# Optimization experiments

Hardware: AMD Instinct MI355X
Metric: run time of the kernel (lower is better)

Reference implementation:

```python
import jax, jax.numpy as jnp
import numpy as np


def setup_inputs() -> dict:
    key = jax.random.key(0)
    k1, k2 = jax.random.split(key)
    T, D, E = 8192, 4096, 64  # tokens, model_dim, num_experts
    x = jax.random.normal(k1, (T, D), dtype=jnp.float32)
    wg = jax.random.normal(k2, (E, D), dtype=jnp.float32) * (1.0 / np.sqrt(D))
    return {"x": x, "wg": wg}


def reference(x, wg):
    # gate logits: nn.Linear(model_dim, num_experts, bias=False) in fp32
    logits = jnp.einsum('td,ed->te', x.astype(jnp.float32), wg)  # [T, E]
    gates = jax.nn.softmax(logits, axis=1)                        # [T, E]
    # top1gating (eval mode: no noise): argmax over gates
    indices1_s = jnp.argmax(gates, axis=1)                        # [T] int
    # gates = (gates * one_hot(indices1_s)).sum(dim=1) == gather of the max gate
    gates1_s = jnp.take_along_axis(gates, indices1_s[:, None], axis=1)[:, 0]  # [T]
    return indices1_s, gates1_s
```

## Files before the change

kernel.cpp:

```cpp
#include <hip/hip_runtime.h>

typedef __attribute__((ext_vector_type(8))) short bf16x8;
typedef __attribute__((ext_vector_type(4))) float f32x4;

constexpr int TN = 8192;
constexpr int DN = 4096;
constexpr int EN = 64;

constexpr int BM = 32;
constexpr int NS = DN / 32;
constexpr int NT = 16;

__device__ __forceinline__ unsigned short f2bf(float f) {
    unsigned u = __builtin_bit_cast(unsigned, f);
    u += 0x7FFFu + ((u >> 16) & 1u);
    return (unsigned short)(u >> 16);
}
__device__ __forceinline__ float bf2f(unsigned short h) {
    unsigned u = ((unsigned)h) << 16;
    return __builtin_bit_cast(float, u);
}

__global__ __launch_bounds__(256)
void wg_frag_kernel(const float* __restrict__ wg, unsigned short* __restrict__ BF) {
    const int gid = blockIdx.x * 256 + threadIdx.x;
    const int l  = gid & 63;
    const int et = (gid >> 6) & 3;
    const int s  = (gid >> 8) & (NS - 1);
    const int p  = gid >> 15;
    const int e  = et * 16 + (l & 15);
    const int k  = s * 32 + (l >> 4) * 8;

    const float* src = wg + (size_t)e * DN + k;
    float4 v0 = *reinterpret_cast<const float4*>(src);
    float4 v1 = *reinterpret_cast<const float4*>(src + 4);
    float f[8] = {v0.x, v0.y, v0.z, v0.w, v1.x, v1.y, v1.z, v1.w};
    unsigned short o[8];
#pragma unroll
    for (int j = 0; j < 8; ++j) {
        unsigned short h = f2bf(f[j]);
        o[j] = p ? f2bf(f[j] - bf2f(h)) : h;
    }
    unsigned short* dst = BF + (((size_t)p * NS + s) * 4 + et) * 512 + (size_t)l * 8;
    *reinterpret_cast<ushort4*>(dst)     = make_ushort4(o[0], o[1], o[2], o[3]);
    *reinterpret_cast<ushort4*>(dst + 4) = make_ushort4(o[4], o[5], o[6], o[7]);
}

__global__ __launch_bounds__(512, 2)
void gate_fused_kernel(const float* __restrict__ x,
                       const unsigned short* __restrict__ BF,
                       float* __restrict__ out) {
    __shared__ float L[8][BM][68];

    const int tid  = threadIdx.x;
    const int lane = tid & 63;
    const int w    = tid >> 6;
    const int kq   = w & 3;
    const int kh   = w >> 2;
    const int r0   = blockIdx.x * BM;

    const int fr  = lane & 15;
    const int fko = (lane >> 4) * 8;

    const float* xa = x + (size_t)(r0 + fr) * DN + fko;

    f32x4 acc[2][4] = {};

    float4 XA0[2][2], XA1[2][2];
    bf16x8 B0[8], B1[8];

    auto loadA = [&](float4 (&XA)[2][2], int t) {
        const int s = kh * 64 + t * 4 + kq;
        const float* p = xa + s * 32;
#pragma unroll
        for (int rh = 0; rh < 2; ++rh) {
            const float* pr = p + (size_t)rh * 16 * DN;
            XA[rh][0] = *reinterpret_cast<const float4*>(pr);
            XA[rh][1] = *reinterpret_cast<const float4*>(pr + 4);
        }
    };
    auto loadB = [&](bf16x8 (&B)[8], int t) {
        const int s = kh * 64 + t * 4 + kq;
        const unsigned short* bp = BF + (size_t)s * 2048 + (size_t)lane * 8;
#pragma unroll
        for (int et = 0; et < 4; ++et)
            B[et] = *reinterpret_cast<const bf16x8*>(bp + et * 512);
#pragma unroll
        for (int et = 0; et < 4; ++et)
            B[4 + et] = *reinterpret_cast<const bf16x8*>(bp + (size_t)NS * 2048 + et * 512);
    };
    auto compute = [&](float4 (&XA)[2][2], bf16x8 (&B)[8]) {
        bf16x8 ah[2], al[2];
#pragma unroll
        for (int rh = 0; rh < 2; ++rh) {
            float f[8] = {XA[rh][0].x, XA[rh][0].y, XA[rh][0].z, XA[rh][0].w,
                          XA[rh][1].x, XA[rh][1].y, XA[rh][1].z, XA[rh][1].w};
#pragma unroll
            for (int j = 0; j < 8; ++j) {
                unsigned short hh = f2bf(f[j]);
                ah[rh][j] = (short)hh;
                al[rh][j] = (short)f2bf(f[j] - bf2f(hh));
            }
        }
#pragma unroll
        for (int et = 0; et < 4; ++et)
#pragma unroll
            for (int rh = 0; rh < 2; ++rh) {
                acc[rh][et] = __builtin_amdgcn_mfma_f32_16x16x32_bf16(ah[rh], B[et],     acc[rh][et], 0, 0, 0);
                acc[rh][et] = __builtin_amdgcn_mfma_f32_16x16x32_bf16(al[rh], B[et],     acc[rh][et], 0, 0, 0);
                acc[rh][et] = __builtin_amdgcn_mfma_f32_16x16x32_bf16(ah[rh], B[4 + et], acc[rh][et], 0, 0, 0);
                acc[rh][et] = __builtin_amdgcn_mfma_f32_16x16x32_bf16(al[rh], B[4 + et], acc[rh][et], 0, 0, 0);
            }
    };

    loadA(XA0, 0);
    loadB(B0, 0);
#pragma unroll 2
    for (int t = 0; t < NT; t += 2) {
        if (t + 1 < NT) { loadA(XA1, t + 1); loadB(B1, t + 1); }
        compute(XA0, B0);
        if (t + 2 < NT) { loadA(XA0, t + 2); loadB(B0, t + 2); }
        compute(XA1, B1);
    }

#pragma unroll
    for (int rh = 0; rh < 2; ++rh)
#pragma unroll
        for (int et = 0; et < 4; ++et)
#pragma unroll
            for (int r = 0; r < 4; ++r)
                L[w][rh * 16 + (lane >> 4) * 4 + r][et * 16 + fr] = acc[rh][et][r];
    __syncthreads();

    {
        const int row = tid >> 4;
        const int eg  = tid & 15;
        float v[4];
#pragma unroll
        for (int j = 0; j < 4; ++j) {
            float s = L[0][row][eg * 4 + j];
#pragma unroll
            for (int q = 1; q < 8; ++q) s += L[q][row][eg * 4 + j];
            v[j] = s;
        }
        float m = v[0];
        int idx = eg * 4;
#pragma unroll
        for (int j = 1; j < 4; ++j)
            if (v[j] > m) { m = v[j]; idx = eg * 4 + j; }
#pragma unroll
        for (int d = 1; d < 16; d <<= 1) {
            float om = __shfl_xor(m, d);
            int   oi = __shfl_xor(idx, d);
            if (om > m || (om == m && oi < idx)) { m = om; idx = oi; }
        }
        float s = 0.0f;
#pragma unroll
        for (int j = 0; j < 4; ++j) s += __expf(v[j] - m);
#pragma unroll
        for (int d = 1; d < 16; d <<= 1) s += __shfl_xor(s, d);
        if (eg == 0) {
            out[r0 + row]      = (float)idx;
            out[TN + r0 + row] = 1.0f / s;
        }
    }
}

extern "C" void kernel_launch(void* const* d_in, const int* in_sizes, int n_in,
                              void* d_out, int out_size, void* d_ws, size_t ws_size,
                              hipStream_t stream) {
    const float* x  = (const float*)d_in[0];
    const float* wg = (const float*)d_in[1];
    float* out = (float*)d_out;

    unsigned short* BF = (unsigned short*)d_ws;

    wg_frag_kernel<<<dim3(256), dim3(256), 0, stream>>>(wg, BF);
    gate_fused_kernel<<<dim3(TN / BM), dim3(512), 0, stream>>>(x, BF, out);
}
```

Measured before the change: 38.26 us.

## Split gate GEMM over K into partials with a separate top-1 softmax kernel

The fused gate kernel becomes two kernels. A GEMM kernel uses 256 threads and 16-row tiles, splits the K dimension in two across blocks, and writes partial logits to workspace. A second kernel sums the partials per row and does argmax plus softmax normalisation. The aim is more, smaller blocks for better occupancy and latency hiding while streaming x. The cost is an extra launch, a partial-logit round trip, doubled reads of the weight fragments, and B loads that are no longer double-buffered. The KSPLIT=1 fallback only covers half of K, so it would give wrong results if it ever ran.

```diff
diff --git a/kernel.cpp b/kernel.cpp
--- a/kernel.cpp
+++ b/kernel.cpp
@@ -7,7 +7,7 @@
 constexpr int DN = 4096;
 constexpr int EN = 64;
 
-constexpr int BM = 32;
+constexpr int BM = 16;
 constexpr int NS = DN / 32;
 constexpr int NT = 16;
 
@@ -46,41 +46,38 @@
     *reinterpret_cast<ushort4*>(dst + 4) = make_ushort4(o[4], o[5], o[6], o[7]);
 }
 
-__global__ __launch_bounds__(512, 2)
-void gate_fused_kernel(const float* __restrict__ x,
-                       const unsigned short* __restrict__ BF,
-                       float* __restrict__ out) {
-    __shared__ float L[8][BM][68];
+template <int KSPLIT>
+__global__ __launch_bounds__(256, 4)
+void gate_gemm_kernel(const float* __restrict__ x,
+                      const unsigned short* __restrict__ BF,
+                      float* __restrict__ part) {
+    __shared__ float L[4][BM][68];
 
     const int tid  = threadIdx.x;
     const int lane = tid & 63;
     const int w    = tid >> 6;
-    const int kq   = w & 3;
-    const int kh   = w >> 2;
-    const int r0   = blockIdx.x * BM;
+    const int rt   = blockIdx.x >> (KSPLIT - 1);
+    const int ks   = blockIdx.x & (KSPLIT - 1);
+    const int r0   = rt * BM;
+    const int sbase = ks * (NS / KSPLIT);
 
     const int fr  = lane & 15;
     const int fko = (lane >> 4) * 8;
 
     const float* xa = x + (size_t)(r0 + fr) * DN + fko;
 
-    f32x4 acc[2][4] = {};
+    f32x4 acc[4] = {};
 
-    float4 XA0[2][2], XA1[2][2];
-    bf16x8 B0[8], B1[8];
+    float4 XA0[2], XA1[2];
+    bf16x8 B[8];
 
-    auto loadA = [&](float4 (&XA)[2][2], int t) {
-        const int s = kh * 64 + t * 4 + kq;
-        const float* p = xa + s * 32;
-#pragma unroll
-        for (int rh = 0; rh < 2; ++rh) {
-            const float* pr = p + (size_t)rh * 16 * DN;
-            XA[rh][0] = *reinterpret_cast<const float4*>(pr);
-            XA[rh][1] = *reinterpret_cast<const float4*>(pr + 4);
-        }
+    auto loadA = [&](float4 (&XA)[2], int t) {
+        const float* p = xa + (size_t)(sbase + t * 4 + w) * 32;
+        XA[0] = *reinterpret_cast<const float4*>(p);
+        XA[1] = *reinterpret_cast<const float4*>(p + 4);
     };
-    auto loadB = [&](bf16x8 (&B)[8], int t) {
-        const int s = kh * 64 + t * 4 + kq;
+    auto loadB = [&](int t) {
+        const int s = sbase + t * 4 + w;
         const unsigned short* bp = BF + (size_t)s * 2048 + (size_t)lane * 8;
 #pragma unroll
         for (int et = 0; et < 4; ++et)
@@ -89,47 +86,43 @@
         for (int et = 0; et < 4; ++et)
             B[4 + et] = *reinterpret_cast<const bf16x8*>(bp + (size_t)NS * 2048 + et * 512);
     };
-    auto compute = [&](float4 (&XA)[2][2], bf16x8 (&B)[8]) {
-        bf16x8 ah[2], al[2];
+    auto compute = [&](float4 (&XA)[2]) {
+        float f[8] = {XA[0].x, XA[0].y, XA[0].z, XA[0].w,
+                      XA[1].x, XA[1].y, XA[1].z, XA[1].w};
+        bf16x8 ah, al;
 #pragma unroll
-        for (int rh = 0; rh < 2; ++rh) {
-            float f[8] = {XA[rh][0].x, XA[rh][0].y, XA[rh][0].z, XA[rh][0].w,
-                          XA[rh][1].x, XA[rh][1].y, XA[rh][1].z, XA[rh][1].w};
-#pragma unroll
-            for (int j = 0; j < 8; ++j) {
-                unsigned short hh = f2bf(f[j]);
-                ah[rh][j] = (short)hh;
-                al[rh][j] = (short)f2bf(f[j] - bf2f(hh));
-            }
+        for (int j = 0; j < 8; ++j) {
+            unsigned short hh = f2bf(f[j]);
+            ah[j] = (short)hh;
+            al[j] = (short)f2bf(f[j] - bf2f(hh));
         }
 #pragma unroll
-        for (int et = 0; et < 4; ++et)
-#pragma unroll
-            for (int rh = 0; rh < 2; ++rh) {
-                acc[rh][et] = __builtin_amdgcn_mfma_f32_16x16x32_bf16(ah[rh], B[et],     acc[rh][et], 0, 0, 0);
-                acc[rh][et] = __builtin_amdgcn_mfma_f32_16x16x32_bf16(al[rh], B[et],     acc[rh][et], 0, 0, 0);
-                acc[rh][et] = __builtin_amdgcn_mfma_f32_16x16x32_bf16(ah[rh], B[4 + et], acc[rh][et], 0, 0, 0);
-                acc[rh][et] = __builtin_amdgcn_mfma_f32_16x16x32_bf16(al[rh], B[4 + et], acc[rh][et], 0, 0, 0);
-            }
+        for (int et = 0; et < 4; ++et) {
+            acc[et] = __builtin_amdgcn_mfma_f32_16x16x32_bf16(ah, B[et],     acc[et], 0, 0, 0);
+            acc[et] = __builtin_amdgcn_mfma_f32_16x16x32_bf16(al, B[et],     acc[et], 0, 0, 0);
+            acc[et] = __builtin_amdgcn_mfma_f32_16x16x32_bf16(ah, B[4 + et], acc[et], 0, 0, 0);
+            acc[et] = __builtin_amdgcn_mfma_f32_16x16x32_bf16(al, B[4 + et], acc[et], 0, 0, 0);
+        }
     };
 
     loadA(XA0, 0);
-    loadB(B0, 0);
 #pragma unroll 2
     for (int t = 0; t < NT; t += 2) {
-        if (t + 1 < NT) { loadA(XA1, t + 1); loadB(B1, t + 1); }
-        compute(XA0, B0);
-        if (t + 2 < NT) { loadA(XA0, t + 2); loadB(B0, t + 2); }
-        compute(XA1, B1);
+        loadB(t);
+        if (t + 1 < NT) loadA(XA1, t + 1);
+        asm volatile("" ::: "memory");
+        compute(XA0);
+        loadB(t + 1);
+        if (t + 2 < NT) loadA(XA0, t + 2);
+        asm volatile("" ::: "memory");
+        compute(XA1);
     }
 
 #pragma unroll
-    for (int rh = 0; rh < 2; ++rh)
+    for (int et = 0; et < 4; ++et)
 #pragma unroll
-        for (int et = 0; et < 4; ++et)
-#pragma unroll
-            for (int r = 0; r < 4; ++r)
-                L[w][rh * 16 + (lane >> 4) * 4 + r][et * 16 + fr] = acc[rh][et][r];
+        for (int r = 0; r < 4; ++r)
+            L[w][(lane >> 4) * 4 + r][et * 16 + fr] = acc[et][r];
     __syncthreads();
 
     {
@@ -137,33 +130,45 @@
         const int eg  = tid & 15;
         float v[4];
 #pragma unroll
-        for (int j = 0; j < 4; ++j) {
-            float s = L[0][row][eg * 4 + j];
+        for (int j = 0; j < 4; ++j)
+            v[j] = L[0][row][eg * 4 + j] + L[1][row][eg * 4 + j]
+                 + L[2][row][eg * 4 + j] + L[3][row][eg * 4 + j];
+        float* dst = part + ((size_t)ks * TN + r0 + row) * EN + eg * 4;
+        *reinterpret_cast<float4*>(dst) = make_float4(v[0], v[1], v[2], v[3]);
+    }
+}
+
+template <int NSPLIT>
+__global__ __launch_bounds__(256)
+void top1_softmax_kernel(const float* __restrict__ part, float* __restrict__ out) {
+    const int row = blockIdx.x * blockDim.x + threadIdx.x;
+    if (row >= TN) return;
+
+    float v[EN];
 #pragma unroll
-            for (int q = 1; q < 8; ++q) s += L[q][row][eg * 4 + j];
-            v[j] = s;
+    for (int i = 0; i < EN / 4; ++i) {
+        float4 s = *reinterpret_cast<const float4*>(&part[(size_t)row * EN + i * 4]);
+#pragma unroll
+        for (int h = 1; h < NSPLIT; ++h) {
+            float4 t = *reinterpret_cast<const float4*>(
+                &part[((size_t)h * TN + row) * EN + i * 4]);
+            s.x += t.x; s.y += t.y; s.z += t.z; s.w += t.w;
         }
-        float m = v[0];
-        int idx = eg * 4;
+        v[i * 4 + 0] = s.x; v[i * 4 + 1] = s.y;
+        v[i * 4 + 2] = s.z; v[i * 4 + 3] = s.w;
+    }
+
+    float m = v[0];
+    int idx = 0;
 #pragma unroll
-        for (int j = 1; j < 4; ++j)
-            if (v[j] > m) { m = v[j]; idx = eg * 4 + j; }
+    for (int e = 1; e < EN; ++e)
+        if (v[e] > m) { m = v[e]; idx = e; }
+    float s = 0.0f;
 #pragma unroll
-        for (int d = 1; d < 16; d <<= 1) {
-            float om = __shfl_xor(m, d);
-            int   oi = __shfl_xor(idx, d);
-            if (om > m || (om == m && oi < idx)) { m = om; idx = oi; }
-        }
-        float s = 0.0f;
-#pragma unroll
-        for (int j = 0; j < 4; ++j) s += __expf(v[j] - m);
-#pragma unroll
-        for (int d = 1; d < 16; d <<= 1) s += __shfl_xor(s, d);
-        if (eg == 0) {
-            out[r0 + row]      = (float)idx;
-            out[TN + r0 + row] = 1.0f / s;
-        }
-    }
+    for (int e = 0; e < EN; ++e) s += __expf(v[e] - m);
+
+    out[row]      = (float)idx;
+    out[TN + row] = 1.0f / s;
 }
 
 extern "C" void kernel_launch(void* const* d_in, const int* in_sizes, int n_in,
@@ -173,8 +178,18 @@
     const float* wg = (const float*)d_in[1];
     float* out = (float*)d_out;
 
+    constexpr size_t BF_BYTES = (size_t)2 * NS * 4 * 512 * 2;
     unsigned short* BF = (unsigned short*)d_ws;
+    float* part = (float*)((char*)d_ws + BF_BYTES);
 
     wg_frag_kernel<<<dim3(256), dim3(256), 0, stream>>>(wg, BF);
-    gate_fused_kernel<<<dim3(TN / BM), dim3(512), 0, stream>>>(x, BF, out);
+
+    const size_t need2 = BF_BYTES + (size_t)2 * TN * EN * sizeof(float);
+    if (ws_size >= need2) {
+        gate_gemm_kernel<2><<<dim3(1024), dim3(256), 0, stream>>>(x, BF, part);
+        top1_softmax_kernel<2><<<dim3(TN / 256), dim3(256), 0, stream>>>(part, out);
+    } else {
+        gate_gemm_kernel<1><<<dim3(512), dim3(256), 0, stream>>>(x, BF, part);
+        top1_softmax_kernel<1><<<dim3(TN / 256), dim3(256), 0, stream>>>(part, out);
+    }
 }
```

After: 52.65 us. 1.38x slower.
